# Kernel tuning notes

Hardware: AMD Instinct MI355X
Metric: run time of the kernel (lower is better)

Reference implementation:

```python
import jax, jax.numpy as jnp
import numpy as np

N_NODES = 100000
N_EDGES = 1000000
F_DIM = 128


def setup_inputs() -> dict:
    key = jax.random.key(0)
    ks = jax.random.split(key, 12)
    s = lambda k, shape: jax.random.normal(k, shape, dtype=jnp.float32) * (1.0 / np.sqrt(shape[0]))
    return {
        "x": jax.random.normal(ks[0], (N_NODES, F_DIM), dtype=jnp.float32),
        "edge_index": jax.random.randint(ks[1], (2, N_EDGES), 0, N_NODES, dtype=jnp.int64),
        "W1": s(ks[2], (2 * F_DIM, 64)), "b1": jnp.zeros((64,), jnp.float32), "A1": s(ks[3], (2 * F_DIM, 64)),
        "W2": s(ks[4], (64, 32)), "b2": jnp.zeros((32,), jnp.float32), "A2": s(ks[5], (64, 32)),
        "W3": s(ks[6], (32, 16)), "b3": jnp.zeros((16,), jnp.float32), "A3": s(ks[7], (32, 16)),
        "Wf": s(ks[8], (16, 1)), "bf": jnp.zeros((1,), jnp.float32),
    }


def _res_block(h, W, b, A):
    # out = relu(h @ W + b); residual = h @ A (bias-free adjust); return relu(out + residual)
    out = jax.nn.relu(h @ W + b)
    return jax.nn.relu(out + h @ A)


def reference(x, edge_index, W1, b1, A1, W2, b2, A2, W3, b3, A3, Wf, bf):
    # NOTE: in the original forward, the GNN output is overwritten by data.x,
    # so the effective computation is gather -> concat -> residual MLP -> sigmoid.
    src, dst = edge_index[0], edge_index[1]
    h = jnp.concatenate([x[src], x[dst]], axis=-1)  # [E, 2F]
    h = _res_block(h, W1, b1, A1)  # [E, 64]
    h = _res_block(h, W2, b2, A2)  # [E, 32]
    h = _res_block(h, W3, b3, A3)  # [E, 16]
    return jax.nn.sigmoid(h @ Wf + bf)  # [E, 1]
```

## Files before the change

kernel.cpp:

```cpp
#include <hip/hip_runtime.h>
#include <stdint.h>
#include <stddef.h>

#define E_TOTAL 1000000
#define N_NODES 100000
#define FD      128
#define ETILE   64
#define NTILES  (E_TOTAL / ETILE)
#define GRID    1024

typedef __attribute__((ext_vector_type(8))) short short8;
typedef __attribute__((ext_vector_type(4))) int   i32x4;
typedef __attribute__((ext_vector_type(4))) float f32x4;

__device__ __forceinline__ short f2bf(float f) {
  union { float f; unsigned u; } v; v.f = f;
  unsigned r = (v.u + 0x7FFFu + ((v.u >> 16) & 1u)) >> 16;
  return (short)(r & 0xFFFFu);
}

__global__ __launch_bounds__(256, 2)
void linkpred_kernel(const float* __restrict__ x,
                     const int* __restrict__ ei,
                     const float* __restrict__ W1, const float* __restrict__ b1,
                     const float* __restrict__ A1,
                     const float* __restrict__ W2, const float* __restrict__ b2,
                     const float* __restrict__ A2,
                     const float* __restrict__ W3, const float* __restrict__ b3,
                     const float* __restrict__ A3,
                     const float* __restrict__ Wf, const float* __restrict__ bfp,
                     float* __restrict__ out)
{
  __shared__ __align__(16) short H0[ETILE][264];
  __shared__ __align__(16) short H1[ETILE][72];
  __shared__ __align__(16) short H2[ETILE][40];

  const int tid  = threadIdx.x;
  const int w    = tid >> 6;
  const int lane = tid & 63;
  const int col  = lane & 15;
  const int quad = lane >> 4;

  short8 B1f[2][8];
  for (int p = 0; p < 2; ++p) {
    const int n = 16 * (w + 4 * p) + col;
    const float* src = (p == 0) ? (W1 + n) : (A1 + (n - 64));
    for (int kt = 0; kt < 8; ++kt) {
      short8 f;
      for (int j = 0; j < 8; ++j)
        f[j] = f2bf(src[(kt * 32 + quad * 8 + j) * 64]);
      B1f[p][kt] = f;
    }
  }
  short8 B2f[2][2];
  for (int p = 0; p < 2; ++p) {
    const int n = 16 * ((w & 1) + 2 * p) + col;
    const float* src = (p == 0) ? (W2 + n) : (A2 + (n - 32));
    for (int kt = 0; kt < 2; ++kt) {
      short8 f;
      for (int j = 0; j < 8; ++j)
        f[j] = f2bf(src[(kt * 32 + quad * 8 + j) * 32]);
      B2f[p][kt] = f;
    }
  }
  short8 B3f[2];
  for (int p = 0; p < 2; ++p) {
    const int n = 16 * p + col;
    const float* src = (p == 0) ? (W3 + n) : (A3 + (n - 16));
    short8 f;
    for (int j = 0; j < 8; ++j)
      f[j] = f2bf(src[(quad * 8 + j) * 16]);
    B3f[p] = f;
  }
  const float b1v = b1[16 * w + col];
  const float b2v = b2[16 * (w & 1) + col];
  const float b3v = b3[col];
  const float bfv = bfp[0];
  const float Wfv = Wf[col];
  const f32x4 zero = {0.f, 0.f, 0.f, 0.f};

  int   nd[8];
  i32x4 gA[8], gB[8];

  auto load_ei = [&](int tile) {
    const int e0 = tile * ETILE;
#pragma unroll
    for (int it = 0; it < 8; ++it) {
      const int h = w * 32 + it * 4 + quad;
      nd[it] = ei[(h & 1) * E_TOTAL + e0 + (h >> 1)];
    }
  };
  auto xissue = [&]() {
#pragma unroll
    for (int it = 0; it < 8; ++it) {
      const float* p = x + (size_t)nd[it] * FD + col * 8;
      asm volatile("global_load_dwordx4 %0, %2, off\n\t"
                   "global_load_dwordx4 %1, %2, off offset:16"
                   : "=&v"(gA[it]), "=&v"(gB[it]) : "v"(p) : "memory");
    }
  };
  auto commit = [&]() {
    asm volatile("s_waitcnt vmcnt(0)" ::: "memory");
    __builtin_amdgcn_sched_barrier(0);
#pragma unroll
    for (int it = 0; it < 8; ++it) {
      const int h    = w * 32 + it * 4 + quad;
      const int e    = h >> 1;
      const int half = h & 1;
      short8 s;
      s[0] = f2bf(__int_as_float(gA[it][0])); s[1] = f2bf(__int_as_float(gA[it][1]));
      s[2] = f2bf(__int_as_float(gA[it][2])); s[3] = f2bf(__int_as_float(gA[it][3]));
      s[4] = f2bf(__int_as_float(gB[it][0])); s[5] = f2bf(__int_as_float(gB[it][1]));
      s[6] = f2bf(__int_as_float(gB[it][2])); s[7] = f2bf(__int_as_float(gB[it][3]));
      *(short8*)&H0[e][half * 128 + col * 8] = s;
    }
  };

  load_ei(blockIdx.x);
  xissue();
  if (blockIdx.x + (int)gridDim.x < NTILES) load_ei(blockIdx.x + gridDim.x);

  for (int tile = blockIdx.x; tile < NTILES; tile += gridDim.x) {
    const int e0 = tile * ETILE;

    commit();
    __syncthreads();

    const int nx = tile + gridDim.x;
    if (nx < NTILES) xissue();
    if (nx + (int)gridDim.x < NTILES) load_ei(nx + gridDim.x);

    for (int mt = 0; mt < 4; ++mt) {
      f32x4 a0 = zero, a1 = zero;
      for (int kt = 0; kt < 8; ++kt) {
        short8 a = *(const short8*)&H0[mt * 16 + col][kt * 32 + quad * 8];
        a0 = __builtin_amdgcn_mfma_f32_16x16x32_bf16(a, B1f[0][kt], a0, 0, 0, 0);
        a1 = __builtin_amdgcn_mfma_f32_16x16x32_bf16(a, B1f[1][kt], a1, 0, 0, 0);
      }
      for (int r = 0; r < 4; ++r) {
        float o = fmaxf(a0[r] + b1v, 0.f);
        float h = fmaxf(o + a1[r], 0.f);
        H1[mt * 16 + quad * 4 + r][16 * w + col] = f2bf(h);
      }
    }
    __syncthreads();

    for (int mi = 0; mi < 2; ++mi) {
      f32x4 a0 = zero, a1 = zero;
      const int m = (2 * (w >> 1) + mi) * 16 + col;
      for (int kt = 0; kt < 2; ++kt) {
        short8 a = *(const short8*)&H1[m][kt * 32 + quad * 8];
        a0 = __builtin_amdgcn_mfma_f32_16x16x32_bf16(a, B2f[0][kt], a0, 0, 0, 0);
        a1 = __builtin_amdgcn_mfma_f32_16x16x32_bf16(a, B2f[1][kt], a1, 0, 0, 0);
      }
      for (int r = 0; r < 4; ++r) {
        float o = fmaxf(a0[r] + b2v, 0.f);
        float h = fmaxf(o + a1[r], 0.f);
        H2[(2 * (w >> 1) + mi) * 16 + quad * 4 + r][16 * (w & 1) + col] = f2bf(h);
      }
    }
    __syncthreads();

    f32x4 acc3[2];
    acc3[0] = zero; acc3[1] = zero;
    {
      short8 a = *(const short8*)&H2[w * 16 + col][quad * 8];
      acc3[0] = __builtin_amdgcn_mfma_f32_16x16x32_bf16(a, B3f[0], acc3[0], 0, 0, 0);
      acc3[1] = __builtin_amdgcn_mfma_f32_16x16x32_bf16(a, B3f[1], acc3[1], 0, 0, 0);
    }

#pragma unroll
    for (int r = 0; r < 4; ++r) {
      float o = fmaxf(acc3[0][r] + b3v, 0.f);
      float h = fmaxf(o + acc3[1][r], 0.f);
      float t = h * Wfv;
      t += __shfl_xor(t, 1, 16);
      t += __shfl_xor(t, 2, 16);
      t += __shfl_xor(t, 4, 16);
      t += __shfl_xor(t, 8, 16);
      if (col == r) {
        float s = bfv + t;
        out[e0 + w * 16 + quad * 4 + r] = 1.0f / (1.0f + __expf(-s));
      }
    }
  }
}

extern "C" void kernel_launch(void* const* d_in, const int* in_sizes, int n_in,
                              void* d_out, int out_size, void* d_ws, size_t ws_size,
                              hipStream_t stream) {
  const float* x   = (const float*)d_in[0];
  const int*   ei  = (const int*)d_in[1];
  const float* W1  = (const float*)d_in[2];
  const float* b1  = (const float*)d_in[3];
  const float* A1  = (const float*)d_in[4];
  const float* W2  = (const float*)d_in[5];
  const float* b2  = (const float*)d_in[6];
  const float* A2  = (const float*)d_in[7];
  const float* W3  = (const float*)d_in[8];
  const float* b3  = (const float*)d_in[9];
  const float* A3  = (const float*)d_in[10];
  const float* Wf  = (const float*)d_in[11];
  const float* bfp = (const float*)d_in[12];

  hipLaunchKernelGGL(linkpred_kernel, dim3(GRID), dim3(256), 0, stream,
                     x, ei, W1, b1, A1, W2, b2, A2, W3, b3, A3, Wf, bfp,
                     (float*)d_out);
}
```

Measured before the change: 284.4 us.

## Drop software prefetch pipeline, raise occupancy, swizzle and alias LDS buffers

Removes the register-held prefetch of the next tile's gathered rows and edge indices, and instead gathers synchronously in two batches per tile. LDS padding is replaced by XOR swizzles, and the layer-2 and layer-3 buffers are aliased into one array, which needs an extra barrier. These changes shrink register and LDS use so the kernel can run four blocks per CU with twice the grid. The goal is to hide gather latency through occupancy rather than explicit prefetch. The risk is that latency is no longer overlapped within a block.

```diff
diff --git a/kernel.cpp b/kernel.cpp
--- a/kernel.cpp
+++ b/kernel.cpp
@@ -7,10 +7,9 @@
 #define FD      128
 #define ETILE   64
 #define NTILES  (E_TOTAL / ETILE)
-#define GRID    1024
+#define GRID    2048
 
 typedef __attribute__((ext_vector_type(8))) short short8;
-typedef __attribute__((ext_vector_type(4))) int   i32x4;
 typedef __attribute__((ext_vector_type(4))) float f32x4;
 
 __device__ __forceinline__ short f2bf(float f) {
@@ -19,7 +18,14 @@
   return (short)(r & 0xFFFFu);
 }
 
-__global__ __launch_bounds__(256, 2)
+__device__ __forceinline__ int h0idx(int row, int c8) {
+  return row * 256 + (c8 ^ ((row & 7) << 3));
+}
+__device__ __forceinline__ int h1idx(int row, int c) {
+  return row * 64 + (c ^ (((row >> 1) & 7) << 3));
+}
+
+__global__ __launch_bounds__(256, 4)
 void linkpred_kernel(const float* __restrict__ x,
                      const int* __restrict__ ei,
                      const float* __restrict__ W1, const float* __restrict__ b1,
@@ -31,9 +37,8 @@
                      const float* __restrict__ Wf, const float* __restrict__ bfp,
                      float* __restrict__ out)
 {
-  __shared__ __align__(16) short H0[ETILE][264];
-  __shared__ __align__(16) short H1[ETILE][72];
-  __shared__ __align__(16) short H2[ETILE][40];
+  __shared__ __align__(16) short H0[ETILE * 256];
+  __shared__ __align__(16) short H12[ETILE * 64];
 
   const int tid  = threadIdx.x;
   const int w    = tid >> 6;
@@ -79,92 +84,69 @@
   const float Wfv = Wf[col];
   const f32x4 zero = {0.f, 0.f, 0.f, 0.f};
 
-  int   nd[8];
-  i32x4 gA[8], gB[8];
-
-  auto load_ei = [&](int tile) {
-    const int e0 = tile * ETILE;
-#pragma unroll
-    for (int it = 0; it < 8; ++it) {
-      const int h = w * 32 + it * 4 + quad;
-      nd[it] = ei[(h & 1) * E_TOTAL + e0 + (h >> 1)];
-    }
-  };
-  auto xissue = [&]() {
-#pragma unroll
-    for (int it = 0; it < 8; ++it) {
-      const float* p = x + (size_t)nd[it] * FD + col * 8;
-      asm volatile("global_load_dwordx4 %0, %2, off\n\t"
-                   "global_load_dwordx4 %1, %2, off offset:16"
-                   : "=&v"(gA[it]), "=&v"(gB[it]) : "v"(p) : "memory");
-    }
-  };
-  auto commit = [&]() {
-    asm volatile("s_waitcnt vmcnt(0)" ::: "memory");
-    __builtin_amdgcn_sched_barrier(0);
-#pragma unroll
-    for (int it = 0; it < 8; ++it) {
-      const int h    = w * 32 + it * 4 + quad;
-      const int e    = h >> 1;
-      const int half = h & 1;
-      short8 s;
-      s[0] = f2bf(__int_as_float(gA[it][0])); s[1] = f2bf(__int_as_float(gA[it][1]));
-      s[2] = f2bf(__int_as_float(gA[it][2])); s[3] = f2bf(__int_as_float(gA[it][3]));
-      s[4] = f2bf(__int_as_float(gB[it][0])); s[5] = f2bf(__int_as_float(gB[it][1]));
-      s[6] = f2bf(__int_as_float(gB[it][2])); s[7] = f2bf(__int_as_float(gB[it][3]));
-      *(short8*)&H0[e][half * 128 + col * 8] = s;
-    }
-  };
-
-  load_ei(blockIdx.x);
-  xissue();
-  if (blockIdx.x + (int)gridDim.x < NTILES) load_ei(blockIdx.x + gridDim.x);
-
   for (int tile = blockIdx.x; tile < NTILES; tile += gridDim.x) {
     const int e0 = tile * ETILE;
 
-    commit();
+    for (int b = 0; b < 2; ++b) {
+      int nd[4];
+#pragma unroll
+      for (int it = 0; it < 4; ++it) {
+        const int h = w * 32 + (b * 4 + it) * 4 + quad;
+        nd[it] = ei[(h & 1) * E_TOTAL + e0 + (h >> 1)];
+      }
+#pragma unroll
+      for (int it = 0; it < 4; ++it) {
+        const int h = w * 32 + (b * 4 + it) * 4 + quad;
+        const float4* s4 = ((const float4*)(x + (size_t)nd[it] * FD)) + col * 2;
+        float4 va = s4[0];
+        float4 vb = s4[1];
+        short8 s;
+        s[0] = f2bf(va.x); s[1] = f2bf(va.y); s[2] = f2bf(va.z); s[3] = f2bf(va.w);
+        s[4] = f2bf(vb.x); s[5] = f2bf(vb.y); s[6] = f2bf(vb.z); s[7] = f2bf(vb.w);
+        *(short8*)&H0[h0idx(h >> 1, (h & 1) * 128 + col * 8)] = s;
+      }
+    }
     __syncthreads();
-
-    const int nx = tile + gridDim.x;
-    if (nx < NTILES) xissue();
-    if (nx + (int)gridDim.x < NTILES) load_ei(nx + gridDim.x);
 
     for (int mt = 0; mt < 4; ++mt) {
       f32x4 a0 = zero, a1 = zero;
       for (int kt = 0; kt < 8; ++kt) {
-        short8 a = *(const short8*)&H0[mt * 16 + col][kt * 32 + quad * 8];
+        short8 a = *(const short8*)&H0[h0idx(mt * 16 + col, kt * 32 + quad * 8)];
         a0 = __builtin_amdgcn_mfma_f32_16x16x32_bf16(a, B1f[0][kt], a0, 0, 0, 0);
         a1 = __builtin_amdgcn_mfma_f32_16x16x32_bf16(a, B1f[1][kt], a1, 0, 0, 0);
       }
       for (int r = 0; r < 4; ++r) {
         float o = fmaxf(a0[r] + b1v, 0.f);
         float h = fmaxf(o + a1[r], 0.f);
-        H1[mt * 16 + quad * 4 + r][16 * w + col] = f2bf(h);
+        H12[h1idx(mt * 16 + quad * 4 + r, 16 * w + col)] = f2bf(h);
       }
     }
     __syncthreads();
 
+    f32x4 c2w[2], c2a[2];
+    c2w[0] = zero; c2w[1] = zero; c2a[0] = zero; c2a[1] = zero;
     for (int mi = 0; mi < 2; ++mi) {
-      f32x4 a0 = zero, a1 = zero;
       const int m = (2 * (w >> 1) + mi) * 16 + col;
       for (int kt = 0; kt < 2; ++kt) {
-        short8 a = *(const short8*)&H1[m][kt * 32 + quad * 8];
-        a0 = __builtin_amdgcn_mfma_f32_16x16x32_bf16(a, B2f[0][kt], a0, 0, 0, 0);
-        a1 = __builtin_amdgcn_mfma_f32_16x16x32_bf16(a, B2f[1][kt], a1, 0, 0, 0);
-      }
-      for (int r = 0; r < 4; ++r) {
-        float o = fmaxf(a0[r] + b2v, 0.f);
-        float h = fmaxf(o + a1[r], 0.f);
-        H2[(2 * (w >> 1) + mi) * 16 + quad * 4 + r][16 * (w & 1) + col] = f2bf(h);
+        short8 a = *(const short8*)&H12[h1idx(m, kt * 32 + quad * 8)];
+        c2w[mi] = __builtin_amdgcn_mfma_f32_16x16x32_bf16(a, B2f[0][kt], c2w[mi], 0, 0, 0);
+        c2a[mi] = __builtin_amdgcn_mfma_f32_16x16x32_bf16(a, B2f[1][kt], c2a[mi], 0, 0, 0);
       }
     }
+    __syncthreads();
+
+    for (int mi = 0; mi < 2; ++mi)
+      for (int r = 0; r < 4; ++r) {
+        float o = fmaxf(c2w[mi][r] + b2v, 0.f);
+        float h = fmaxf(o + c2a[mi][r], 0.f);
+        H12[((2 * (w >> 1) + mi) * 16 + quad * 4 + r) * 40 + 16 * (w & 1) + col] = f2bf(h);
+      }
     __syncthreads();
 
     f32x4 acc3[2];
     acc3[0] = zero; acc3[1] = zero;
     {
-      short8 a = *(const short8*)&H2[w * 16 + col][quad * 8];
+      short8 a = *(const short8*)&H12[(w * 16 + col) * 40 + quad * 8];
       acc3[0] = __builtin_amdgcn_mfma_f32_16x16x32_bf16(a, B3f[0], acc3[0], 0, 0, 0);
       acc3[1] = __builtin_amdgcn_mfma_f32_16x16x32_bf16(a, B3f[1], acc3[1], 0, 0, 0);
     }
```

Result: slower. 376.7 us (+32.4%).
